# Performance work log

Hardware: AMD Instinct MI355X
Metric: run time of the kernel (lower is better)

The kernel has to match this reference:

```python
import jax, jax.numpy as jnp
import numpy as np

N_DOCS = 500_000
VOCAB = 30522
NNZ_PER_DOC = 64
NNZ = N_DOCS * NNZ_PER_DOC
Q_NNZ = 64
TOP_K = 10


def setup_inputs() -> dict:
    key = jax.random.key(0)
    k1, k2, k3, k4 = jax.random.split(key, 4)
    # sparse query in COO form: [1, q_nnz] indices into vocab, [1, q_nnz] values
    indices = jax.random.randint(k1, (1, Q_NNZ), 0, VOCAB, dtype=jnp.int32)
    values = jax.random.normal(k2, (1, Q_NNZ), dtype=jnp.float32)
    # CSR collection matrix [N_DOCS, VOCAB], fixed nnz per row for generation
    crow = jnp.arange(N_DOCS + 1, dtype=jnp.int32) * NNZ_PER_DOC
    col = jax.random.randint(k3, (NNZ,), 0, VOCAB, dtype=jnp.int32)
    vals = jax.random.normal(k4, (NNZ,), dtype=jnp.float32) * 0.1
    return {"indices": indices, "values": values, "crow": crow, "col": col, "vals": vals}


def reference(indices, values, crow, col, vals):
    # densify sparse COO query (duplicates sum, matching to_dense of uncoalesced COO)
    query = jnp.zeros((VOCAB,), jnp.float32).at[indices[0]].add(values[0])
    # CSR SpMV: per-nnz contribution = vals * query[col], segment-sum by row
    nnz = vals.shape[0]
    row_ids = jnp.searchsorted(crow, jnp.arange(nnz, dtype=crow.dtype), side="right") - 1
    contrib = vals * query[col]
    scores = jax.ops.segment_sum(contrib, row_ids, num_segments=N_DOCS)  # [N_DOCS]
    top_vals, top_idx = jax.lax.top_k(scores, TOP_K)
    return top_vals, top_idx
```

## Files before the change

### kernel.cpp

```cpp
#include <hip/hip_runtime.h>
#include <math.h>

constexpr int VOCAB      = 30522;
constexpr int N_DOCS     = 500000;
constexpr int NNZ_ROW    = 64;
constexpr int Q_NNZ      = 64;
constexpr int TOP_K      = 10;
constexpr int BM_WORDS   = (VOCAB + 31) / 32;

constexpr int SPMV_BLOCKS  = 2048;
constexpr int TOPK_BLOCKS  = 128;

__global__ void build_query(const int* __restrict__ qidx,
                            const float* __restrict__ qval,
                            float* __restrict__ qdense) {
    if (blockIdx.x == 0 && threadIdx.x == 0) {
        for (int i = 0; i < Q_NNZ; ++i) qdense[qidx[i]] = 0.0f;
        for (int i = 0; i < Q_NNZ; ++i) qdense[qidx[i]] += qval[i];
    }
}

__global__ __launch_bounds__(256) void spmv(const int* __restrict__ qidx,
                                            const float* __restrict__ qdense,
                                            const int* __restrict__ col,
                                            const float* __restrict__ vals,
                                            float* __restrict__ scores) {
    __shared__ unsigned bm[BM_WORDS];
    for (int i = threadIdx.x; i < BM_WORDS; i += blockDim.x) bm[i] = 0u;
    __syncthreads();
    if (threadIdx.x < Q_NNZ) {
        int c = qidx[threadIdx.x];
        atomicOr(&bm[c >> 5], 1u << (c & 31));
    }
    __syncthreads();

    const int lane   = threadIdx.x & 63;
    const int waveid = threadIdx.x >> 6;
    const int grp    = lane >> 4;
    const int lin    = lane & 15;

    const int ntiles = N_DOCS / 16;
    for (int tile = blockIdx.x; tile < ntiles; tile += gridDim.x) {
        const int row  = tile * 16 + waveid * 4 + grp;
        const int base = row * NNZ_ROW + lin * 4;

        const int4 c4 = *reinterpret_cast<const int4*>(col + base);

        float acc = 0.0f;
        { int c = c4.x; if ((bm[c >> 5] >> (c & 31)) & 1u) acc += vals[base + 0] * qdense[c]; }
        { int c = c4.y; if ((bm[c >> 5] >> (c & 31)) & 1u) acc += vals[base + 1] * qdense[c]; }
        { int c = c4.z; if ((bm[c >> 5] >> (c & 31)) & 1u) acc += vals[base + 2] * qdense[c]; }
        { int c = c4.w; if ((bm[c >> 5] >> (c & 31)) & 1u) acc += vals[base + 3] * qdense[c]; }

        acc += __shfl_xor(acc, 1);
        acc += __shfl_xor(acc, 2);
        acc += __shfl_xor(acc, 4);
        acc += __shfl_xor(acc, 8);

        if (lin == 0) scores[row] = acc;
    }
}

__device__ __forceinline__ void lds_merge_tree(float* sv, int* si, int t) {
    for (int s = 128; s >= 1; s >>= 1) {
        if (t < s) {
            const int a = t * TOP_K, b = (t + s) * TOP_K;
            float mv[TOP_K]; int mi[TOP_K];
            int i = 0, j = 0;
#pragma unroll
            for (int k = 0; k < TOP_K; ++k) {
                float av = sv[a + i], bv = sv[b + j];
                int   ai = si[a + i], bi = si[b + j];
                bool ta = (av > bv) || (av == bv && ai <= bi);
                mv[k] = ta ? av : bv;
                mi[k] = ta ? ai : bi;
                if (ta) ++i; else ++j;
            }
#pragma unroll
            for (int k = 0; k < TOP_K; ++k) { sv[a + k] = mv[k]; si[a + k] = mi[k]; }
        }
        __syncthreads();
    }
}

__global__ __launch_bounds__(256) void topk_partial(const float* __restrict__ scores,
                                                    float* __restrict__ cand_v,
                                                    int* __restrict__ cand_i) {
    float tv[TOP_K]; int ti[TOP_K];
#pragma unroll
    for (int k = 0; k < TOP_K; ++k) { tv[k] = -INFINITY; ti[k] = 0x7fffffff; }

    const int tid    = blockIdx.x * blockDim.x + threadIdx.x;
    const int stride = gridDim.x * blockDim.x;
    for (int i = tid; i < N_DOCS; i += stride) {
        float v = scores[i];
        if (v > tv[TOP_K - 1] || (v == tv[TOP_K - 1] && i < ti[TOP_K - 1])) {
            int vi = i;
#pragma unroll
            for (int k = 0; k < TOP_K; ++k) {
                bool better = (v > tv[k]) || (v == tv[k] && vi < ti[k]);
                if (better) {
                    float a = tv[k]; int b = ti[k];
                    tv[k] = v; ti[k] = vi;
                    v = a; vi = b;
                }
            }
        }
    }

    __shared__ float sv[256 * TOP_K];
    __shared__ int   si[256 * TOP_K];
    const int t = threadIdx.x;
#pragma unroll
    for (int k = 0; k < TOP_K; ++k) { sv[t * TOP_K + k] = tv[k]; si[t * TOP_K + k] = ti[k]; }
    __syncthreads();

    lds_merge_tree(sv, si, t);

    if (t == 0) {
        for (int k = 0; k < TOP_K; ++k) {
            cand_v[blockIdx.x * TOP_K + k] = sv[k];
            cand_i[blockIdx.x * TOP_K + k] = si[k];
        }
    }
}

__global__ __launch_bounds__(256) void topk_final(const float* __restrict__ cand_v,
                                                  const int* __restrict__ cand_i,
                                                  float* __restrict__ out,
                                                  int nlists) {
    __shared__ float sv[256 * TOP_K];
    __shared__ int   si[256 * TOP_K];
    const int t = threadIdx.x;
    if (t < nlists) {
        for (int k = 0; k < TOP_K; ++k) {
            sv[t * TOP_K + k] = cand_v[t * TOP_K + k];
            si[t * TOP_K + k] = cand_i[t * TOP_K + k];
        }
    } else {
        for (int k = 0; k < TOP_K; ++k) {
            sv[t * TOP_K + k] = -INFINITY;
            si[t * TOP_K + k] = 0x7fffffff;
        }
    }
    __syncthreads();

    lds_merge_tree(sv, si, t);

    if (t == 0) {
        for (int k = 0; k < TOP_K; ++k) {
            out[k]         = sv[k];
            out[TOP_K + k] = (float)si[k];
        }
    }
}

extern "C" void kernel_launch(void* const* d_in, const int* in_sizes, int n_in,
                              void* d_out, int out_size, void* d_ws, size_t ws_size,
                              hipStream_t stream) {
    const int*   qidx = (const int*)  d_in[0];
    const float* qval = (const float*)d_in[1];
    const int*   col  = (const int*)  d_in[3];
    const float* vals = (const float*)d_in[4];
    float* out = (float*)d_out;

    char* ws = (char*)d_ws;
    float* qdense = (float*)ws;
    size_t off = (size_t)((VOCAB * 4 + 127) & ~127);
    float* scores = (float*)(ws + off);
    off += (size_t)N_DOCS * 4;
    float* cand_v = (float*)(ws + off);
    off += (size_t)TOPK_BLOCKS * TOP_K * 4;
    int* cand_i = (int*)(ws + off);

    build_query<<<1, 64, 0, stream>>>(qidx, qval, qdense);
    spmv<<<SPMV_BLOCKS, 256, 0, stream>>>(qidx, qdense, col, vals, scores);
    topk_partial<<<TOPK_BLOCKS, 256, 0, stream>>>(scores, cand_v, cand_i);
    topk_final<<<1, 256, 0, stream>>>(cand_v, cand_i, out, TOPK_BLOCKS);
}
```

Before: 77.52 us.

## Fuse SpMV with per-block top-k and drop the scores buffer

Merges the SpMV and partial top-k kernels so each block keeps its row scores in shared memory and emits a local top-10 candidate list, removing the global scores write and re-read plus one launch. The SpMV lane mapping changes to 4 lanes per row with four non-temporal int4 column loads each, and build_query now runs in parallel across 64 threads. The final merge scans all 2048 block candidate lists with early exit. The entry buffer assumes at most 4 passes per wave, which is tied to the grid size constants.

```diff
diff --git a/kernel.cpp b/kernel.cpp
--- a/kernel.cpp
+++ b/kernel.cpp
@@ -1,68 +1,33 @@
 #include <hip/hip_runtime.h>
 #include <math.h>
 
-constexpr int VOCAB      = 30522;
-constexpr int N_DOCS     = 500000;
-constexpr int NNZ_ROW    = 64;
-constexpr int Q_NNZ      = 64;
-constexpr int TOP_K      = 10;
-constexpr int BM_WORDS   = (VOCAB + 31) / 32;
-
-constexpr int SPMV_BLOCKS  = 2048;
-constexpr int TOPK_BLOCKS  = 128;
-
-__global__ void build_query(const int* __restrict__ qidx,
-                            const float* __restrict__ qval,
-                            float* __restrict__ qdense) {
-    if (blockIdx.x == 0 && threadIdx.x == 0) {
-        for (int i = 0; i < Q_NNZ; ++i) qdense[qidx[i]] = 0.0f;
-        for (int i = 0; i < Q_NNZ; ++i) qdense[qidx[i]] += qval[i];
-    }
-}
-
-__global__ __launch_bounds__(256) void spmv(const int* __restrict__ qidx,
-                                            const float* __restrict__ qdense,
-                                            const int* __restrict__ col,
-                                            const float* __restrict__ vals,
-                                            float* __restrict__ scores) {
-    __shared__ unsigned bm[BM_WORDS];
-    for (int i = threadIdx.x; i < BM_WORDS; i += blockDim.x) bm[i] = 0u;
-    __syncthreads();
-    if (threadIdx.x < Q_NNZ) {
-        int c = qidx[threadIdx.x];
-        atomicOr(&bm[c >> 5], 1u << (c & 31));
-    }
-    __syncthreads();
-
-    const int lane   = threadIdx.x & 63;
-    const int waveid = threadIdx.x >> 6;
-    const int grp    = lane >> 4;
-    const int lin    = lane & 15;
-
-    const int ntiles = N_DOCS / 16;
-    for (int tile = blockIdx.x; tile < ntiles; tile += gridDim.x) {
-        const int row  = tile * 16 + waveid * 4 + grp;
-        const int base = row * NNZ_ROW + lin * 4;
-
-        const int4 c4 = *reinterpret_cast<const int4*>(col + base);
-
-        float acc = 0.0f;
-        { int c = c4.x; if ((bm[c >> 5] >> (c & 31)) & 1u) acc += vals[base + 0] * qdense[c]; }
-        { int c = c4.y; if ((bm[c >> 5] >> (c & 31)) & 1u) acc += vals[base + 1] * qdense[c]; }
-        { int c = c4.z; if ((bm[c >> 5] >> (c & 31)) & 1u) acc += vals[base + 2] * qdense[c]; }
-        { int c = c4.w; if ((bm[c >> 5] >> (c & 31)) & 1u) acc += vals[base + 3] * qdense[c]; }
-
-        acc += __shfl_xor(acc, 1);
-        acc += __shfl_xor(acc, 2);
-        acc += __shfl_xor(acc, 4);
-        acc += __shfl_xor(acc, 8);
-
-        if (lin == 0) scores[row] = acc;
-    }
-}
-
-__device__ __forceinline__ void lds_merge_tree(float* sv, int* si, int t) {
-    for (int s = 128; s >= 1; s >>= 1) {
+constexpr int VOCAB    = 30522;
+constexpr int N_DOCS   = 500000;
+constexpr int Q_NNZ    = 64;
+constexpr int TOP_K    = 10;
+constexpr int BM_WORDS = (VOCAB + 31) / 32;
+
+constexpr int SPMV_BLOCKS = 2048;
+constexpr int NTILES      = N_DOCS / 16;
+constexpr int WAVES_TOTAL = SPMV_BLOCKS * 4;
+constexpr int MAX_PASSES  = (NTILES + WAVES_TOTAL - 1) / WAVES_TOTAL;
+
+typedef int int4v __attribute__((ext_vector_type(4)));
+
+__device__ __forceinline__ void topk_insert(float (&tv)[TOP_K], int (&ti)[TOP_K],
+                                            float v, int vi) {
+    if (v > tv[TOP_K - 1] || (v == tv[TOP_K - 1] && vi < ti[TOP_K - 1])) {
+#pragma unroll
+        for (int k = 0; k < TOP_K; ++k) {
+            bool better = (v > tv[k]) || (v == tv[k] && vi < ti[k]);
+            if (better) { float a = tv[k]; int b = ti[k]; tv[k] = v; ti[k] = vi; v = a; vi = b; }
+        }
+    }
+}
+
+template <int S0>
+__device__ void merge_tree(float* sv, int* si, int t) {
+    for (int s = S0; s >= 1; s >>= 1) {
         if (t < s) {
             const int a = t * TOP_K, b = (t + s) * TOP_K;
             float mv[TOP_K]; int mi[TOP_K];
@@ -83,69 +48,134 @@
     }
 }
 
-__global__ __launch_bounds__(256) void topk_partial(const float* __restrict__ scores,
-                                                    float* __restrict__ cand_v,
-                                                    int* __restrict__ cand_i) {
-    float tv[TOP_K]; int ti[TOP_K];
-#pragma unroll
-    for (int k = 0; k < TOP_K; ++k) { tv[k] = -INFINITY; ti[k] = 0x7fffffff; }
-
-    const int tid    = blockIdx.x * blockDim.x + threadIdx.x;
-    const int stride = gridDim.x * blockDim.x;
-    for (int i = tid; i < N_DOCS; i += stride) {
-        float v = scores[i];
-        if (v > tv[TOP_K - 1] || (v == tv[TOP_K - 1] && i < ti[TOP_K - 1])) {
-            int vi = i;
-#pragma unroll
-            for (int k = 0; k < TOP_K; ++k) {
-                bool better = (v > tv[k]) || (v == tv[k] && vi < ti[k]);
-                if (better) {
-                    float a = tv[k]; int b = ti[k];
-                    tv[k] = v; ti[k] = vi;
-                    v = a; vi = b;
-                }
-            }
-        }
-    }
-
+__global__ void build_query(const int* __restrict__ qidx,
+                            const float* __restrict__ qval,
+                            float* __restrict__ qdense) {
+    __shared__ int   sidx[Q_NNZ];
+    __shared__ float sval[Q_NNZ];
+    const int i = threadIdx.x;
+    sidx[i] = qidx[i];
+    sval[i] = qval[i];
+    __syncthreads();
+    const int qi = sidx[i];
+    float s = 0.0f;
+    for (int j = 0; j < Q_NNZ; ++j)
+        if (sidx[j] == qi) s += sval[j];
+    qdense[qi] = s;
+}
+
+__global__ __launch_bounds__(256) void spmv_topk(const int* __restrict__ qidx,
+                                                 const float* __restrict__ qdense,
+                                                 const int* __restrict__ col,
+                                                 const float* __restrict__ vals,
+                                                 float* __restrict__ cand_v,
+                                                 int* __restrict__ cand_i) {
+    __shared__ unsigned bm[BM_WORDS];
+    __shared__ float ent_v[256];
+    __shared__ int   ent_i[256];
+    __shared__ float sv[64 * TOP_K];
+    __shared__ int   si[64 * TOP_K];
+
+    for (int i = threadIdx.x; i < BM_WORDS; i += 256) bm[i] = 0u;
+    ent_v[threadIdx.x] = -INFINITY;
+    ent_i[threadIdx.x] = 0x7fffffff;
+    __syncthreads();
+    if (threadIdx.x < Q_NNZ) {
+        int c = qidx[threadIdx.x];
+        atomicOr(&bm[c >> 5], 1u << (c & 31));
+    }
+    __syncthreads();
+
+    const int lane   = threadIdx.x & 63;
+    const int waveid = threadIdx.x >> 6;
+    const int grp    = lane >> 2;
+    const int lin    = lane & 3;
+
+    const int gwave = blockIdx.x * 4 + waveid;
+
+    int pass = 0;
+    for (int tile = gwave; tile < NTILES; tile += WAVES_TOTAL, ++pass) {
+        const int row = tile * 16 + grp;
+        const size_t base = (size_t)row * 64 + (size_t)(lin * 4);
+
+        const int4v c0 = __builtin_nontemporal_load((const int4v*)(col + base));
+        const int4v c1 = __builtin_nontemporal_load((const int4v*)(col + base + 16));
+        const int4v c2 = __builtin_nontemporal_load((const int4v*)(col + base + 32));
+        const int4v c3 = __builtin_nontemporal_load((const int4v*)(col + base + 48));
+
+        float acc = 0.0f;
+#define PROC1(c, off) { int cc = (c); if ((bm[cc >> 5] >> (cc & 31)) & 1u) \
+                            acc += vals[base + (off)] * qdense[cc]; }
+#define PROC4(cv, off) PROC1((cv).x, (off)+0) PROC1((cv).y, (off)+1) \
+                       PROC1((cv).z, (off)+2) PROC1((cv).w, (off)+3)
+        PROC4(c0, 0)
+        PROC4(c1, 16)
+        PROC4(c2, 32)
+        PROC4(c3, 48)
+#undef PROC4
+#undef PROC1
+
+        acc += __shfl_xor(acc, 1);
+        acc += __shfl_xor(acc, 2);
+
+        if (lin == 0) {
+            const int slot = (pass * 4 + waveid) * 16 + grp;
+            ent_v[slot] = acc;
+            ent_i[slot] = row;
+        }
+    }
+    __syncthreads();
+
+    const int t = threadIdx.x;
+    if (t < 64) {
+        float tv[TOP_K]; int ti[TOP_K];
+#pragma unroll
+        for (int k = 0; k < TOP_K; ++k) { tv[k] = -INFINITY; ti[k] = 0x7fffffff; }
+#pragma unroll
+        for (int r = 0; r < 4; ++r)
+            topk_insert(tv, ti, ent_v[t + r * 64], ent_i[t + r * 64]);
+#pragma unroll
+        for (int k = 0; k < TOP_K; ++k) { sv[t * TOP_K + k] = tv[k]; si[t * TOP_K + k] = ti[k]; }
+    }
+    __syncthreads();
+
+    merge_tree<32>(sv, si, t);
+
+    if (t == 0) {
+        for (int k = 0; k < TOP_K; ++k) {
+            cand_v[blockIdx.x * TOP_K + k] = sv[k];
+            cand_i[blockIdx.x * TOP_K + k] = si[k];
+        }
+    }
+}
+
+__global__ __launch_bounds__(256) void topk_final(const float* __restrict__ cand_v,
+                                                  const int* __restrict__ cand_i,
+                                                  float* __restrict__ out) {
     __shared__ float sv[256 * TOP_K];
     __shared__ int   si[256 * TOP_K];
     const int t = threadIdx.x;
+
+    float tv[TOP_K]; int ti[TOP_K];
+#pragma unroll
+    for (int k = 0; k < TOP_K; ++k) { tv[k] = -INFINITY; ti[k] = 0x7fffffff; }
+
+    for (int r = 0; r < SPMV_BLOCKS / 256; ++r) {
+        const int b = t + r * 256;
+#pragma unroll
+        for (int k = 0; k < TOP_K; ++k) {
+            float v  = cand_v[b * TOP_K + k];
+            int   vi = cand_i[b * TOP_K + k];
+            if (!(v > tv[TOP_K - 1] || (v == tv[TOP_K - 1] && vi < ti[TOP_K - 1]))) break;
+            topk_insert(tv, ti, v, vi);
+        }
+    }
+
 #pragma unroll
     for (int k = 0; k < TOP_K; ++k) { sv[t * TOP_K + k] = tv[k]; si[t * TOP_K + k] = ti[k]; }
     __syncthreads();
 
-    lds_merge_tree(sv, si, t);
-
-    if (t == 0) {
-        for (int k = 0; k < TOP_K; ++k) {
-            cand_v[blockIdx.x * TOP_K + k] = sv[k];
-            cand_i[blockIdx.x * TOP_K + k] = si[k];
-        }
-    }
-}
-
-__global__ __launch_bounds__(256) void topk_final(const float* __restrict__ cand_v,
-                                                  const int* __restrict__ cand_i,
-                                                  float* __restrict__ out,
-                                                  int nlists) {
-    __shared__ float sv[256 * TOP_K];
-    __shared__ int   si[256 * TOP_K];
-    const int t = threadIdx.x;
-    if (t < nlists) {
-        for (int k = 0; k < TOP_K; ++k) {
-            sv[t * TOP_K + k] = cand_v[t * TOP_K + k];
-            si[t * TOP_K + k] = cand_i[t * TOP_K + k];
-        }
-    } else {
-        for (int k = 0; k < TOP_K; ++k) {
-            sv[t * TOP_K + k] = -INFINITY;
-            si[t * TOP_K + k] = 0x7fffffff;
-        }
-    }
-    __syncthreads();
-
-    lds_merge_tree(sv, si, t);
+    merge_tree<128>(sv, si, t);
 
     if (t == 0) {
         for (int k = 0; k < TOP_K; ++k) {
@@ -167,14 +197,11 @@
     char* ws = (char*)d_ws;
     float* qdense = (float*)ws;
     size_t off = (size_t)((VOCAB * 4 + 127) & ~127);
-    float* scores = (float*)(ws + off);
-    off += (size_t)N_DOCS * 4;
     float* cand_v = (float*)(ws + off);
-    off += (size_t)TOPK_BLOCKS * TOP_K * 4;
+    off += (size_t)SPMV_BLOCKS * TOP_K * 4;
     int* cand_i = (int*)(ws + off);
 
-    build_query<<<1, 64, 0, stream>>>(qidx, qval, qdense);
-    spmv<<<SPMV_BLOCKS, 256, 0, stream>>>(qidx, qdense, col, vals, scores);
-    topk_partial<<<TOPK_BLOCKS, 256, 0, stream>>>(scores, cand_v, cand_i);
-    topk_final<<<1, 256, 0, stream>>>(cand_v, cand_i, out, TOPK_BLOCKS);
-}
+    build_query<<<1, Q_NNZ, 0, stream>>>(qidx, qval, qdense);
+    spmv_topk<<<SPMV_BLOCKS, 256, 0, stream>>>(qidx, qdense, col, vals, cand_v, cand_i);
+    topk_final<<<1, 256, 0, stream>>>(cand_v, cand_i, out);
+}
```

Result: slower. 94.24 us (+21.6%).

## Stream nnz flatly with sparse atomic score updates instead of per-row reduction

Applied to the files above, without the earlier changes.

The row-tiled SpMV, which used a 16-lane shuffle reduction per row, is replaced by a flat grid-stride stream over the column array in 4-wide vectors. A thread reads vals and does an atomicAdd into its row's score only when one of its columns hits the query bitmap, which should be rare. This drops the shuffles and the per-row score stores and unrolls the loop to keep more loads in flight. In exchange it needs a separate kernel launch to zero the scores, and the dense query build is parallelised across 64 threads. The top-k scan now compares values only before inserting, which still gives the lowest index on ties because each thread scans indices in ascending order.

```diff
diff --git a/kernel.cpp b/kernel.cpp
--- a/kernel.cpp
+++ b/kernel.cpp
@@ -1,68 +1,32 @@
 #include <hip/hip_runtime.h>
 #include <math.h>
 
-constexpr int VOCAB      = 30522;
-constexpr int N_DOCS     = 500000;
-constexpr int NNZ_ROW    = 64;
-constexpr int Q_NNZ      = 64;
-constexpr int TOP_K      = 10;
-constexpr int BM_WORDS   = (VOCAB + 31) / 32;
+constexpr int       VOCAB    = 30522;
+constexpr int       N_DOCS   = 500000;
+constexpr long long NNZ      = (long long)N_DOCS * 64;
+constexpr int       Q_NNZ    = 64;
+constexpr int       TOP_K    = 10;
+constexpr int       BM_WORDS = (VOCAB + 31) / 32;
 
-constexpr int SPMV_BLOCKS  = 2048;
-constexpr int TOPK_BLOCKS  = 128;
+constexpr int STREAM_BLOCKS = 2048;
+constexpr int TOPK_BLOCKS   = 128;
 
-__global__ void build_query(const int* __restrict__ qidx,
-                            const float* __restrict__ qval,
-                            float* __restrict__ qdense) {
-    if (blockIdx.x == 0 && threadIdx.x == 0) {
-        for (int i = 0; i < Q_NNZ; ++i) qdense[qidx[i]] = 0.0f;
-        for (int i = 0; i < Q_NNZ; ++i) qdense[qidx[i]] += qval[i];
+typedef int int4v __attribute__((ext_vector_type(4)));
+
+__device__ __forceinline__ void topk_insert(float (&tv)[TOP_K], int (&ti)[TOP_K],
+                                            float v, int vi) {
+    if (v > tv[TOP_K - 1] || (v == tv[TOP_K - 1] && vi < ti[TOP_K - 1])) {
+#pragma unroll
+        for (int k = 0; k < TOP_K; ++k) {
+            bool better = (v > tv[k]) || (v == tv[k] && vi < ti[k]);
+            if (better) { float a = tv[k]; int b = ti[k]; tv[k] = v; ti[k] = vi; v = a; vi = b; }
+        }
     }
 }
 
-__global__ __launch_bounds__(256) void spmv(const int* __restrict__ qidx,
-                                            const float* __restrict__ qdense,
-                                            const int* __restrict__ col,
-                                            const float* __restrict__ vals,
-                                            float* __restrict__ scores) {
-    __shared__ unsigned bm[BM_WORDS];
-    for (int i = threadIdx.x; i < BM_WORDS; i += blockDim.x) bm[i] = 0u;
-    __syncthreads();
-    if (threadIdx.x < Q_NNZ) {
-        int c = qidx[threadIdx.x];
-        atomicOr(&bm[c >> 5], 1u << (c & 31));
-    }
-    __syncthreads();
-
-    const int lane   = threadIdx.x & 63;
-    const int waveid = threadIdx.x >> 6;
-    const int grp    = lane >> 4;
-    const int lin    = lane & 15;
-
-    const int ntiles = N_DOCS / 16;
-    for (int tile = blockIdx.x; tile < ntiles; tile += gridDim.x) {
-        const int row  = tile * 16 + waveid * 4 + grp;
-        const int base = row * NNZ_ROW + lin * 4;
-
-        const int4 c4 = *reinterpret_cast<const int4*>(col + base);
-
-        float acc = 0.0f;
-        { int c = c4.x; if ((bm[c >> 5] >> (c & 31)) & 1u) acc += vals[base + 0] * qdense[c]; }
-        { int c = c4.y; if ((bm[c >> 5] >> (c & 31)) & 1u) acc += vals[base + 1] * qdense[c]; }
-        { int c = c4.z; if ((bm[c >> 5] >> (c & 31)) & 1u) acc += vals[base + 2] * qdense[c]; }
-        { int c = c4.w; if ((bm[c >> 5] >> (c & 31)) & 1u) acc += vals[base + 3] * qdense[c]; }
-
-        acc += __shfl_xor(acc, 1);
-        acc += __shfl_xor(acc, 2);
-        acc += __shfl_xor(acc, 4);
-        acc += __shfl_xor(acc, 8);
-
-        if (lin == 0) scores[row] = acc;
-    }
-}
-
-__device__ __forceinline__ void lds_merge_tree(float* sv, int* si, int t) {
-    for (int s = 128; s >= 1; s >>= 1) {
+template <int S0>
+__device__ void merge_tree(float* sv, int* si, int t) {
+    for (int s = S0; s >= 1; s >>= 1) {
         if (t < s) {
             const int a = t * TOP_K, b = (t + s) * TOP_K;
             float mv[TOP_K]; int mi[TOP_K];
@@ -83,6 +47,64 @@
     }
 }
 
+__global__ __launch_bounds__(256) void zero_scores(float4* __restrict__ s) {
+    const int i = blockIdx.x * 256 + threadIdx.x;
+    if (i < N_DOCS / 4) s[i] = float4{0.0f, 0.0f, 0.0f, 0.0f};
+}
+
+__global__ void build_query(const int* __restrict__ qidx,
+                            const float* __restrict__ qval,
+                            float* __restrict__ qdense) {
+    __shared__ int   sidx[Q_NNZ];
+    __shared__ float sval[Q_NNZ];
+    const int i = threadIdx.x;
+    sidx[i] = qidx[i];
+    sval[i] = qval[i];
+    __syncthreads();
+    const int qi = sidx[i];
+    float s = 0.0f;
+    for (int j = 0; j < Q_NNZ; ++j)
+        if (sidx[j] == qi) s += sval[j];
+    qdense[qi] = s;
+}
+
+__global__ __launch_bounds__(256) void spmv_stream(const int* __restrict__ qidx,
+                                                   const float* __restrict__ qdense,
+                                                   const int* __restrict__ col,
+                                                   const float* __restrict__ vals,
+                                                   float* __restrict__ scores) {
+    __shared__ unsigned bm[BM_WORDS];
+    for (int i = threadIdx.x; i < BM_WORDS; i += 256) bm[i] = 0u;
+    __syncthreads();
+    if (threadIdx.x < Q_NNZ) {
+        int c = qidx[threadIdx.x];
+        atomicOr(&bm[c >> 5], 1u << (c & 31));
+    }
+    __syncthreads();
+
+    const long long nvec   = NNZ / 4;
+    const long long stride = (long long)STREAM_BLOCKS * 256;
+
+#pragma unroll 4
+    for (long long v = (long long)blockIdx.x * 256 + threadIdx.x; v < nvec; v += stride) {
+        const int4v c4 = *(const int4v*)(col + v * 4);
+
+        const unsigned h0 = (bm[(unsigned)c4.x >> 5] >> (c4.x & 31)) & 1u;
+        const unsigned h1 = (bm[(unsigned)c4.y >> 5] >> (c4.y & 31)) & 1u;
+        const unsigned h2 = (bm[(unsigned)c4.z >> 5] >> (c4.z & 31)) & 1u;
+        const unsigned h3 = (bm[(unsigned)c4.w >> 5] >> (c4.w & 31)) & 1u;
+
+        if (h0 | h1 | h2 | h3) {
+            float s = 0.0f;
+            if (h0) s += vals[v * 4 + 0] * qdense[c4.x];
+            if (h1) s += vals[v * 4 + 1] * qdense[c4.y];
+            if (h2) s += vals[v * 4 + 2] * qdense[c4.z];
+            if (h3) s += vals[v * 4 + 3] * qdense[c4.w];
+            atomicAdd(&scores[(int)(v >> 4)], s);
+        }
+    }
+}
+
 __global__ __launch_bounds__(256) void topk_partial(const float* __restrict__ scores,
                                                     float* __restrict__ cand_v,
                                                     int* __restrict__ cand_i) {
@@ -93,19 +115,8 @@
     const int tid    = blockIdx.x * blockDim.x + threadIdx.x;
     const int stride = gridDim.x * blockDim.x;
     for (int i = tid; i < N_DOCS; i += stride) {
-        float v = scores[i];
-        if (v > tv[TOP_K - 1] || (v == tv[TOP_K - 1] && i < ti[TOP_K - 1])) {
-            int vi = i;
-#pragma unroll
-            for (int k = 0; k < TOP_K; ++k) {
-                bool better = (v > tv[k]) || (v == tv[k] && vi < ti[k]);
-                if (better) {
-                    float a = tv[k]; int b = ti[k];
-                    tv[k] = v; ti[k] = vi;
-                    v = a; vi = b;
-                }
-            }
-        }
+        const float v = scores[i];
+        if (v > tv[TOP_K - 1]) topk_insert(tv, ti, v, i);
     }
 
     __shared__ float sv[256 * TOP_K];
@@ -115,7 +126,7 @@
     for (int k = 0; k < TOP_K; ++k) { sv[t * TOP_K + k] = tv[k]; si[t * TOP_K + k] = ti[k]; }
     __syncthreads();
 
-    lds_merge_tree(sv, si, t);
+    merge_tree<128>(sv, si, t);
 
     if (t == 0) {
         for (int k = 0; k < TOP_K; ++k) {
@@ -127,12 +138,12 @@
 
 __global__ __launch_bounds__(256) void topk_final(const float* __restrict__ cand_v,
                                                   const int* __restrict__ cand_i,
-                                                  float* __restrict__ out,
-                                                  int nlists) {
+                                                  float* __restrict__ out) {
     __shared__ float sv[256 * TOP_K];
     __shared__ int   si[256 * TOP_K];
     const int t = threadIdx.x;
-    if (t < nlists) {
+
+    if (t < TOPK_BLOCKS) {
         for (int k = 0; k < TOP_K; ++k) {
             sv[t * TOP_K + k] = cand_v[t * TOP_K + k];
             si[t * TOP_K + k] = cand_i[t * TOP_K + k];
@@ -145,7 +156,7 @@
     }
     __syncthreads();
 
-    lds_merge_tree(sv, si, t);
+    merge_tree<128>(sv, si, t);
 
     if (t == 0) {
         for (int k = 0; k < TOP_K; ++k) {
@@ -165,16 +176,17 @@
     float* out = (float*)d_out;
 
     char* ws = (char*)d_ws;
-    float* qdense = (float*)ws;
-    size_t off = (size_t)((VOCAB * 4 + 127) & ~127);
-    float* scores = (float*)(ws + off);
-    off += (size_t)N_DOCS * 4;
+    float* scores = (float*)ws;
+    size_t off = (size_t)N_DOCS * 4;
+    float* qdense = (float*)(ws + off);
+    off += (size_t)((VOCAB * 4 + 127) & ~127);
     float* cand_v = (float*)(ws + off);
     off += (size_t)TOPK_BLOCKS * TOP_K * 4;
     int* cand_i = (int*)(ws + off);
 
-    build_query<<<1, 64, 0, stream>>>(qidx, qval, qdense);
-    spmv<<<SPMV_BLOCKS, 256, 0, stream>>>(qidx, qdense, col, vals, scores);
+    zero_scores<<<(N_DOCS / 4 + 255) / 256, 256, 0, stream>>>((float4*)scores);
+    build_query<<<1, Q_NNZ, 0, stream>>>(qidx, qval, qdense);
+    spmv_stream<<<STREAM_BLOCKS, 256, 0, stream>>>(qidx, qdense, col, vals, scores);
     topk_partial<<<TOPK_BLOCKS, 256, 0, stream>>>(scores, cand_v, cand_i);
-    topk_final<<<1, 256, 0, stream>>>(cand_v, cand_i, out, TOPK_BLOCKS);
+    topk_final<<<1, 256, 0, stream>>>(cand_v, cand_i, out);
 }
```

After: 73.04 us. -5.8%, faster.
